# Kernel optimization log

Measured on AMD Instinct MI355X. Metric: run time of the kernel, lower is better.

The kernel has to match this reference:

```python
import jax, jax.numpy as jnp
import numpy as np

N = 50000      # nodes
E = 800000     # edges
G = 32         # graphs in batch
K = 16         # max current nodes per graph
F_IN = 128
HID = 64
HEADS = 4
NEG = -1e9
TEMPERATURE = 1.0


def setup_inputs() -> dict:
    key = jax.random.key(0)
    ks = jax.random.split(key, 16)
    inp = {
        "x": jax.random.normal(ks[0], (N, F_IN), dtype=jnp.float32),
        "edge_index": jax.random.randint(ks[1], (2, E), 0, N, dtype=jnp.int64) if jax.config.jax_enable_x64 else jax.random.randint(ks[1], (2, E), 0, N).astype(jnp.int32),
        "cur_nodes": jax.random.randint(ks[2], (G, K), 0, N).astype(jnp.int32),
        "cur_counts": jax.random.randint(ks[3], (G,), 0, K).astype(jnp.int32),
        "masks": jax.random.bernoulli(ks[4], 0.3, (G, N)),
        "W1": jax.random.normal(ks[5], (F_IN, HEADS * HID), dtype=jnp.float32) * 0.05,
        "att_src1": jax.random.normal(ks[6], (HEADS, HID), dtype=jnp.float32) * 0.05,
        "att_dst1": jax.random.normal(ks[7], (HEADS, HID), dtype=jnp.float32) * 0.05,
        "b1": jax.random.normal(ks[8], (HEADS * HID,), dtype=jnp.float32) * 0.05,
        "W2": jax.random.normal(ks[9], (HEADS * HID, HID), dtype=jnp.float32) * 0.05,
        "att_src2": jax.random.normal(ks[10], (1, HID), dtype=jnp.float32) * 0.05,
        "att_dst2": jax.random.normal(ks[11], (1, HID), dtype=jnp.float32) * 0.05,
        "b2": jax.random.normal(ks[12], (HID,), dtype=jnp.float32) * 0.05,
        "action_w": jax.random.normal(ks[13], (HID, 1), dtype=jnp.float32) * 0.01,
        "action_b": jnp.zeros((1,), dtype=jnp.float32),
        "stop_w": jax.random.normal(ks[14], (HID, 1), dtype=jnp.float32) * 0.01,
        "stop_b": jnp.zeros((1,), dtype=jnp.float32),
    }
    return inp


def gat_conv(x, src, dst, W, att_s, att_d, b, num_nodes):
    """PyG-style GATConv (add_self_loops already applied to src/dst)."""
    H, C = att_s.shape
    h = (x @ W).reshape(num_nodes, H, C)            # [N,H,C]
    a_s = jnp.sum(h * att_s[None], axis=-1)         # [N,H]
    a_d = jnp.sum(h * att_d[None], axis=-1)         # [N,H]
    e = jax.nn.leaky_relu(a_s[src] + a_d[dst], 0.2) # [E',H]
    m = jax.ops.segment_max(e, dst, num_segments=num_nodes)
    ex = jnp.exp(e - m[dst])
    denom = jax.ops.segment_sum(ex, dst, num_segments=num_nodes)
    coef = ex / denom[dst]                          # scatter-softmax over dst
    out = jax.ops.segment_sum(coef[:, :, None] * h[src], dst, num_segments=num_nodes)
    return out.reshape(num_nodes, H * C) + b


def reference(x, edge_index, cur_nodes, cur_counts, masks,
              W1, att_src1, att_dst1, b1, W2, att_src2, att_dst2, b2,
              action_w, action_b, stop_w, stop_b):
    num_nodes = x.shape[0]
    loops = jnp.arange(num_nodes, dtype=edge_index.dtype)
    src = jnp.concatenate([edge_index[0], loops])
    dst = jnp.concatenate([edge_index[1], loops])

    h = jax.nn.relu(gat_conv(x, src, dst, W1, att_src1, att_dst1, b1, num_nodes))
    h = gat_conv(h, src, dst, W2, att_src2, att_dst2, b2, num_nodes)  # [N,HID]

    node_scores = jnp.tanh(h @ action_w + action_b)[:, 0]             # [N]

    # per-graph masked gather-mean pooling over current nodes
    valid = (jnp.arange(K)[None, :] < cur_counts[:, None])            # [G,K]
    gathered = h[cur_nodes] * valid[:, :, None].astype(h.dtype)       # [G,K,HID]
    cnt = jnp.maximum(cur_counts, 1).astype(h.dtype)
    contexts = gathered.sum(axis=1) / cnt[:, None]                    # [G,HID]
    stop_scores = jnp.tanh(contexts @ stop_w + stop_b)                # [G,1]

    masked = jnp.where(masks, node_scores[None, :], NEG)              # [G,N]
    all_scores = jnp.concatenate([masked, stop_scores], axis=1) / TEMPERATURE
    probs = jax.nn.softmax(all_scores, axis=-1)                       # [G,N+1]

    stop = (cur_counts == 0)
    onehot = jnp.zeros((num_nodes + 1,), dtype=probs.dtype).at[num_nodes].set(1.0)
    return jnp.where(stop[:, None], onehot[None, :], probs)
```

## Files before the change

kernel.cpp:

```cpp
#include <hip/hip_runtime.h>
#include <hip/hip_runtime_api.h>

#define NNODES 50000
#define NEDGES 800000
#define GG 32
#define KCUR 16
#define FIN 128
#define HIDN 64
#define NHEADS 4
#define F1 256
#define NCHUNK 196
#define NBUCK 196
#define EPB 2048

typedef unsigned short u16;
typedef unsigned char u8;
typedef short bf8 __attribute__((ext_vector_type(8)));
typedef float f32x4 __attribute__((ext_vector_type(4)));
typedef float f32x2 __attribute__((ext_vector_type(2)));

__device__ __forceinline__ u16 f2bf(float f) {
    unsigned u = __float_as_uint(f);
    return (u16)((u + 0x7fffu + ((u >> 16) & 1u)) >> 16);
}
__device__ __forceinline__ float lrelu(float x) { return x > 0.f ? x : 0.2f * x; }
__device__ __forceinline__ unsigned pk4fp8(float a, float b, float c, float d) {
    unsigned u = __builtin_amdgcn_cvt_pk_fp8_f32(a, b, 0u, false);
    u = __builtin_amdgcn_cvt_pk_fp8_f32(c, d, u, true);
    return u;
}

__device__ __forceinline__ void fma16(uint4 hv, float ex, float* acc) {
    f32x2 c;
    c = __builtin_amdgcn_cvt_pk_f32_fp8(hv.x, false);
    acc[0]  = fmaf(ex, c.x, acc[0]);  acc[1]  = fmaf(ex, c.y, acc[1]);
    c = __builtin_amdgcn_cvt_pk_f32_fp8(hv.x, true);
    acc[2]  = fmaf(ex, c.x, acc[2]);  acc[3]  = fmaf(ex, c.y, acc[3]);
    c = __builtin_amdgcn_cvt_pk_f32_fp8(hv.y, false);
    acc[4]  = fmaf(ex, c.x, acc[4]);  acc[5]  = fmaf(ex, c.y, acc[5]);
    c = __builtin_amdgcn_cvt_pk_f32_fp8(hv.y, true);
    acc[6]  = fmaf(ex, c.x, acc[6]);  acc[7]  = fmaf(ex, c.y, acc[7]);
    c = __builtin_amdgcn_cvt_pk_f32_fp8(hv.z, false);
    acc[8]  = fmaf(ex, c.x, acc[8]);  acc[9]  = fmaf(ex, c.y, acc[9]);
    c = __builtin_amdgcn_cvt_pk_f32_fp8(hv.z, true);
    acc[10] = fmaf(ex, c.x, acc[10]); acc[11] = fmaf(ex, c.y, acc[11]);
    c = __builtin_amdgcn_cvt_pk_f32_fp8(hv.w, false);
    acc[12] = fmaf(ex, c.x, acc[12]); acc[13] = fmaf(ex, c.y, acc[13]);
    c = __builtin_amdgcn_cvt_pk_f32_fp8(hv.w, true);
    acc[14] = fmaf(ex, c.x, acc[14]); acc[15] = fmaf(ex, c.y, acc[15]);
}

__device__ __forceinline__ void fma8(uint2 hv, float ex, float* acc) {
    f32x2 c;
    c = __builtin_amdgcn_cvt_pk_f32_fp8(hv.x, false);
    acc[0] = fmaf(ex, c.x, acc[0]); acc[1] = fmaf(ex, c.y, acc[1]);
    c = __builtin_amdgcn_cvt_pk_f32_fp8(hv.x, true);
    acc[2] = fmaf(ex, c.x, acc[2]); acc[3] = fmaf(ex, c.y, acc[3]);
    c = __builtin_amdgcn_cvt_pk_f32_fp8(hv.y, false);
    acc[4] = fmaf(ex, c.x, acc[4]); acc[5] = fmaf(ex, c.y, acc[5]);
    c = __builtin_amdgcn_cvt_pk_f32_fp8(hv.y, true);
    acc[6] = fmaf(ex, c.x, acc[6]); acc[7] = fmaf(ex, c.y, acc[7]);
}

__global__ __launch_bounds__(256)
void pack_k(const float* __restrict__ W1, const float* __restrict__ W2,
            u16* __restrict__ W1p, u16* __restrict__ W2p)
{
    int idx = blockIdx.x * 256 + threadIdx.x;
    const float* src; u16* dst; int S, N, li;
    if (idx < 32768) { src = W1; dst = W1p; S = FIN / 32; N = F1; li = idx; }
    else if (idx < 49152) { src = W2; dst = W2p; S = F1 / 32; N = HIDN; li = idx - 32768; }
    else return;
    int j = li & 7, l = (li >> 3) & 63, rest = li >> 9;
    int s = rest % S, t = rest / S;
    int k = s * 32 + (l >> 4) * 8 + j;
    int n = t * 16 + (l & 15);
    dst[li] = f2bf(src[(size_t)k * N + n]);
}

__global__ __launch_bounds__(256)
void hist_k(const int* __restrict__ dst, int* __restrict__ deg)
{
    int e = blockIdx.x * 256 + threadIdx.x;
    if (e >= NEDGES) return;
    atomicAdd(&deg[dst[e]], 1);
}

__global__ __launch_bounds__(256)
void chunksum_k(const int* __restrict__ deg, int* __restrict__ csum)
{
    __shared__ int ws[4];
    int i = blockIdx.x * 256 + threadIdx.x;
    int v = (i < NNODES) ? deg[i] : 0;
#pragma unroll
    for (int o = 32; o; o >>= 1) v += __shfl_down(v, o);
    if ((threadIdx.x & 63) == 0) ws[threadIdx.x >> 6] = v;
    __syncthreads();
    if (threadIdx.x == 0) csum[blockIdx.x] = ws[0] + ws[1] + ws[2] + ws[3];
}

__global__ __launch_bounds__(256)
void expand_k(const int* __restrict__ deg, const int* __restrict__ csum,
              int* __restrict__ rowptr, int* __restrict__ bcur)
{
    __shared__ int ws[4], ws2[4];
    __shared__ int boff;
    int tid = threadIdx.x, lane = tid & 63, wid = tid >> 6;
    int v0 = (tid < blockIdx.x) ? csum[tid] : 0;
#pragma unroll
    for (int o = 32; o; o >>= 1) v0 += __shfl_down(v0, o);
    if (lane == 0) ws[wid] = v0;
    __syncthreads();
    if (tid == 0) boff = ws[0] + ws[1] + ws[2] + ws[3];
    __syncthreads();
    int i = blockIdx.x * 256 + tid;
    int v = (i < NNODES) ? deg[i] : 0;
    int x = v;
#pragma unroll
    for (int o = 1; o < 64; o <<= 1) {
        int y = __shfl_up(x, o);
        if (lane >= o) x += y;
    }
    if (lane == 63) ws2[wid] = x;
    __syncthreads();
    int off = boff;
    for (int w = 0; w < wid; w++) off += ws2[w];
    int excl = off + x - v;
    if (i < NNODES) {
        rowptr[i] = excl;
        if ((i & 255) == 0) bcur[i >> 8] = excl;
    }
    if (i == 0) rowptr[NNODES] = NEDGES;
}

__global__ __launch_bounds__(256)
void bin_k(const int* __restrict__ src, const int* __restrict__ dst,
           int* __restrict__ bcur, uint2* __restrict__ tmp)
{
    __shared__ int lcnt[NBUCK];
    __shared__ int lbase[NBUCK];
    int tid = threadIdx.x;
    int e0 = blockIdx.x * EPB;
    for (int i = tid; i < NBUCK; i += 256) lcnt[i] = 0;
    __syncthreads();
    int s_[8], d_[8], r_[8];
#pragma unroll
    for (int j = 0; j < 8; j++) {
        int e = e0 + j * 256 + tid;
        if (e < NEDGES) {
            s_[j] = src[e];
            d_[j] = dst[e];
            r_[j] = atomicAdd(&lcnt[d_[j] >> 8], 1);
        }
    }
    __syncthreads();
    for (int i = tid; i < NBUCK; i += 256)
        if (lcnt[i]) lbase[i] = atomicAdd(&bcur[i], lcnt[i]);
    __syncthreads();
#pragma unroll
    for (int j = 0; j < 8; j++) {
        int e = e0 + j * 256 + tid;
        if (e < NEDGES) {
            int b = d_[j] >> 8;
            tmp[lbase[b] + r_[j]] = make_uint2((unsigned)s_[j], (unsigned)d_[j]);
        }
    }
}

__global__ __launch_bounds__(1024)
void reorder_k(const int* __restrict__ rowptr, const uint2* __restrict__ tmp,
               int* __restrict__ csr)
{
    __shared__ int cur[256];
    int tid = threadIdx.x;
    int b = blockIdx.x;
    int n0 = b << 8;
    if (tid < 256) {
        int n = n0 + tid;
        cur[tid] = (n < NNODES) ? rowptr[n] : 0;
    }
    int base = rowptr[n0];
    int end = (b == NBUCK - 1) ? NEDGES : rowptr[n0 + 256];
    __syncthreads();
    for (int e = base + tid; e < end; e += 1024) {
        uint2 pr = tmp[e];
        int pos = atomicAdd(&cur[pr.y & 255], 1);
        csr[pos] = (int)pr.x;
    }
}

__global__ __launch_bounds__(256)
void gemm1_k(const float* __restrict__ X, const u16* __restrict__ Bp,
             const float* __restrict__ att_s, const float* __restrict__ att_d,
             u8* __restrict__ h1f8, float* __restrict__ as1, float* __restrict__ ad1)
{
    const int S = FIN / 32;
    int lane = threadIdx.x & 63, w = threadIdx.x >> 6;
    int m0 = blockIdx.x * 64;
    int row_in = lane & 15, kq = lane >> 4;
    f32x4 acc[4][4];
#pragma unroll
    for (int r = 0; r < 4; r++)
#pragma unroll
        for (int tt = 0; tt < 4; tt++) acc[r][tt] = (f32x4){0.f, 0.f, 0.f, 0.f};
    int R = (NNODES - m0) >> 4; if (R > 4) R = 4;

    for (int s = 0; s < S; s++) {
        bf8 bfrag[4];
#pragma unroll
        for (int tt = 0; tt < 4; tt++) {
            int t = w * 4 + tt;
            bfrag[tt] = *(const bf8*)(Bp + (((size_t)t * S + s) * 64 + lane) * 8);
        }
        int kb = s * 32 + kq * 8;
        bf8 af[4];
#pragma unroll
        for (int r = 0; r < 4; r++)
            if (r < R) {
                const float* xp = X + (size_t)(m0 + r * 16 + row_in) * FIN + kb;
                float4 x0 = *(const float4*)xp;
                float4 x1 = *(const float4*)(xp + 4);
                bf8 a;
                a[0] = (short)f2bf(x0.x); a[1] = (short)f2bf(x0.y);
                a[2] = (short)f2bf(x0.z); a[3] = (short)f2bf(x0.w);
                a[4] = (short)f2bf(x1.x); a[5] = (short)f2bf(x1.y);
                a[6] = (short)f2bf(x1.z); a[7] = (short)f2bf(x1.w);
                af[r] = a;
            }
#pragma unroll
        for (int r = 0; r < 4; r++)
            if (r < R)
#pragma unroll
                for (int tt = 0; tt < 4; tt++)
                    acc[r][tt] = __builtin_amdgcn_mfma_f32_16x16x32_bf16(bfrag[tt], af[r], acc[r][tt], 0, 0, 0);
    }
    float attS[16], attD[16];
#pragma unroll
    for (int tt = 0; tt < 4; tt++)
#pragma unroll
        for (int v = 0; v < 4; v++) {
            attS[tt * 4 + v] = att_s[w * 64 + tt * 16 + kq * 4 + v];
            attD[tt * 4 + v] = att_d[w * 64 + tt * 16 + kq * 4 + v];
        }
#pragma unroll
    for (int r = 0; r < 4; r++) {
        if (r >= R) break;
        int node = m0 + r * 16 + row_in;
        float pa = 0.f, pd = 0.f;
#pragma unroll
        for (int tt = 0; tt < 4; tt++) {
            unsigned u = pk4fp8(acc[r][tt][0], acc[r][tt][1], acc[r][tt][2], acc[r][tt][3]);
            *(unsigned*)(h1f8 + (size_t)node * F1 + (w * 4 + tt) * 16 + kq * 4) = u;
#pragma unroll
            for (int v = 0; v < 4; v++) {
                pa = fmaf(acc[r][tt][v], attS[tt * 4 + v], pa);
                pd = fmaf(acc[r][tt][v], attD[tt * 4 + v], pd);
            }
        }
        pa += __shfl_xor(pa, 16); pa += __shfl_xor(pa, 32);
        pd += __shfl_xor(pd, 16); pd += __shfl_xor(pd, 32);
        if (kq == 0) { as1[node * 4 + w] = pa; ad1[node * 4 + w] = pd; }
    }
}

__global__ __launch_bounds__(256)
void gagg1_gemm2(const int* __restrict__ rowptr, const int* __restrict__ csr,
                 const float* __restrict__ as1, const float* __restrict__ ad1,
                 const u8* __restrict__ h1f8, const float* __restrict__ b1,
                 const u16* __restrict__ W2p,
                 const float* __restrict__ att_s, const float* __restrict__ att_d,
                 u8* __restrict__ h2f8, float* __restrict__ as2, float* __restrict__ ad2)
{
    __shared__ unsigned rows[16 * 128];
    __shared__ float asl[4][16], adl[4][16];
    int tid = threadIdx.x;
    int wid = tid >> 6, lane = tid & 63;
    int q = lane >> 4, li = lane & 15;
    int dl = wid * 4 + q;
    int d0 = blockIdx.x * 16;
    int d = d0 + dl;
    int beg = rowptr[d];
    int tot = rowptr[d + 1] - beg + 1;
    int h = li >> 2;
    int c0 = li << 4;
    const int* rowm = csr + beg - 1;
    float adh = ad1[d * 4 + h];
    float den = 0.f;
    float acc[16];
#pragma unroll
    for (int j = 0; j < 16; j++) acc[j] = 0.f;

    int s0 = d;
    int s1 = (1 < tot) ? rowm[1] : d;
    int s2 = (2 < tot) ? rowm[2] : d;
    int s3 = (3 < tot) ? rowm[3] : d;
    int p = 0;
    while (p < tot) {
        float av0 = as1[((unsigned)s0 << 2) + h];
        float av1 = as1[((unsigned)s1 << 2) + h];
        float av2 = as1[((unsigned)s2 << 2) + h];
        float av3 = as1[((unsigned)s3 << 2) + h];
        uint4 h0 = *(const uint4*)(h1f8 + ((unsigned)s0 << 8) + c0);
        uint4 h1 = *(const uint4*)(h1f8 + ((unsigned)s1 << 8) + c0);
        uint4 h2 = *(const uint4*)(h1f8 + ((unsigned)s2 << 8) + c0);
        uint4 h3 = *(const uint4*)(h1f8 + ((unsigned)s3 << 8) + c0);
        int np = p + 4;
        int n0 = (np     < tot) ? rowm[np]     : d;
        int n1 = (np + 1 < tot) ? rowm[np + 1] : d;
        int n2 = (np + 2 < tot) ? rowm[np + 2] : d;
        int n3 = (np + 3 < tot) ? rowm[np + 3] : d;
        float e0 = __expf(lrelu(av0 + adh));
        float e1 = (p + 1 < tot) ? __expf(lrelu(av1 + adh)) : 0.f;
        float e2 = (p + 2 < tot) ? __expf(lrelu(av2 + adh)) : 0.f;
        float e3 = (p + 3 < tot) ? __expf(lrelu(av3 + adh)) : 0.f;
        den += e0 + e1 + e2 + e3;
        fma16(h0, e0, acc);
        fma16(h1, e1, acc);
        fma16(h2, e2, acc);
        fma16(h3, e3, acc);
        s0 = n0; s1 = n1; s2 = n2; s3 = n3;
        p = np;
    }

    {
        float rden = 1.f / den;
        float4 b0 = *(const float4*)(b1 + c0);
        float4 b4 = *(const float4*)(b1 + c0 + 4);
        float4 b8 = *(const float4*)(b1 + c0 + 8);
        float4 bc = *(const float4*)(b1 + c0 + 12);
        float bb[16] = {b0.x, b0.y, b0.z, b0.w, b4.x, b4.y, b4.z, b4.w,
                        b8.x, b8.y, b8.z, b8.w, bc.x, bc.y, bc.z, bc.w};
        unsigned r[8];
#pragma unroll
        for (int jj = 0; jj < 8; jj++) {
            float lo = fmaxf(fmaf(acc[2 * jj],     rden, bb[2 * jj]),     0.f);
            float hi = fmaxf(fmaf(acc[2 * jj + 1], rden, bb[2 * jj + 1]), 0.f);
            asm("v_cvt_pk_bf16_f32 %0, %1, %2" : "=v"(r[jj]) : "v"(lo), "v"(hi));
        }
        unsigned* rb = rows + dl * 128;
        int g0 = (2 * li) ^ (dl & 7);
        int g1 = (2 * li + 1) ^ (dl & 7);
        *(uint4*)(rb + g0 * 4) = make_uint4(r[0], r[1], r[2], r[3]);
        *(uint4*)(rb + g1 * 4) = make_uint4(r[4], r[5], r[6], r[7]);
    }
    __syncthreads();

    int row_in = li, kq = q;
    f32x4 acc2 = (f32x4){0.f, 0.f, 0.f, 0.f};
#pragma unroll
    for (int s = 0; s < 8; s++) {
        bf8 bfrag = *(const bf8*)(W2p + (((size_t)wid * 8 + s) * 64 + lane) * 8);
        int g = (4 * s + kq) ^ (row_in & 7);
        bf8 af = *(const bf8*)(rows + row_in * 128 + g * 4);
        acc2 = __builtin_amdgcn_mfma_f32_16x16x32_bf16(bfrag, af, acc2, 0, 0, 0);
    }
    int node = d0 + row_in;
    unsigned u = pk4fp8(acc2[0], acc2[1], acc2[2], acc2[3]);
    *(unsigned*)(h2f8 + (size_t)node * HIDN + wid * 16 + kq * 4) = u;
    float pa = 0.f, pd = 0.f;
#pragma unroll
    for (int v = 0; v < 4; v++) {
        pa = fmaf(acc2[v], att_s[wid * 16 + kq * 4 + v], pa);
        pd = fmaf(acc2[v], att_d[wid * 16 + kq * 4 + v], pd);
    }
    pa += __shfl_xor(pa, 16); pa += __shfl_xor(pa, 32);
    pd += __shfl_xor(pd, 16); pd += __shfl_xor(pd, 32);
    if (kq == 0) { asl[wid][row_in] = pa; adl[wid][row_in] = pd; }
    __syncthreads();
    if (tid < 16) {
        as2[d0 + tid] = asl[0][tid] + asl[1][tid] + asl[2][tid] + asl[3][tid];
        ad2[d0 + tid] = adl[0][tid] + adl[1][tid] + adl[2][tid] + adl[3][tid];
    }
}

__global__ __launch_bounds__(256)
void gagg2(const int* __restrict__ rowptr, const int* __restrict__ csr,
           const float* __restrict__ as2, const float* __restrict__ ad2,
           const u8* __restrict__ h2f8, const float* __restrict__ b2,
           const float* __restrict__ aw, const float* __restrict__ ab,
           float* __restrict__ outp, float* __restrict__ scores)
{
    int wid = threadIdx.x >> 6, lane = threadIdx.x & 63;
    int d = blockIdx.x * 4 + wid;
    if (d >= NNODES) return;
    int beg = rowptr[d];
    int tot = rowptr[d + 1] - beg + 1;
    int g8 = lane >> 3;
    int li = lane & 7;
    int c0 = li << 3;
    const int* rowm = csr + beg - 1;
    float adh = ad2[d];
    float den = 0.f;
    float acc[8];
#pragma unroll
    for (int j = 0; j < 8; j++) acc[j] = 0.f;

    int p = g8;
    while (p + 8 < tot) {
        int sa = (p == 0) ? d : rowm[p];
        int sb = rowm[p + 8];
        float ava = as2[sa], avb = as2[sb];
        uint2 ha = *(const uint2*)(h2f8 + ((unsigned)sa << 6) + c0);
        uint2 hb = *(const uint2*)(h2f8 + ((unsigned)sb << 6) + c0);
        float exa = __expf(lrelu(ava + adh));
        den += exa;
        fma8(ha, exa, acc);
        float exb = __expf(lrelu(avb + adh));
        den += exb;
        fma8(hb, exb, acc);
        p += 16;
    }
    if (p < tot) {
        int s = (p == 0) ? d : rowm[p];
        float av = as2[s];
        uint2 hv = *(const uint2*)(h2f8 + ((unsigned)s << 6) + c0);
        float ex = __expf(lrelu(av + adh));
        den += ex;
        fma8(hv, ex, acc);
    }

    den += __shfl_xor(den, 8); den += __shfl_xor(den, 16); den += __shfl_xor(den, 32);
#pragma unroll
    for (int j = 0; j < 8; j++) {
        acc[j] += __shfl_xor(acc[j], 8);
        acc[j] += __shfl_xor(acc[j], 16);
        acc[j] += __shfl_xor(acc[j], 32);
    }

    float rden = 1.f / den;
    float4 blo = *(const float4*)(b2 + c0);
    float4 bhi = *(const float4*)(b2 + c0 + 4);
    float o0 = fmaf(acc[0], rden, blo.x);
    float o1 = fmaf(acc[1], rden, blo.y);
    float o2 = fmaf(acc[2], rden, blo.z);
    float o3 = fmaf(acc[3], rden, blo.w);
    float o4 = fmaf(acc[4], rden, bhi.x);
    float o5 = fmaf(acc[5], rden, bhi.y);
    float o6 = fmaf(acc[6], rden, bhi.z);
    float o7 = fmaf(acc[7], rden, bhi.w);
    if (lane < 8) {
        *(float4*)(outp + (size_t)d * HIDN + c0) = make_float4(o0, o1, o2, o3);
        *(float4*)(outp + (size_t)d * HIDN + c0 + 4) = make_float4(o4, o5, o6, o7);
    }
    float4 alo = *(const float4*)(aw + c0);
    float4 ahi = *(const float4*)(aw + c0 + 4);
    float p_ = o0 * alo.x + o1 * alo.y + o2 * alo.z + o3 * alo.w
             + o4 * ahi.x + o5 * ahi.y + o6 * ahi.z + o7 * ahi.w;
    p_ += __shfl_xor(p_, 1); p_ += __shfl_xor(p_, 2); p_ += __shfl_xor(p_, 4);
    if (lane == 0) scores[d] = tanhf(p_ + ab[0]);
}

__global__ __launch_bounds__(256)
void partials_k(const float* __restrict__ scores, const int* __restrict__ masks,
                float* __restrict__ pmax, float* __restrict__ psum)
{
    __shared__ float lm[4], ls[4];
    int g = blockIdx.y;
    float m = -3.0e38f, s = 0.f;
    for (int n = blockIdx.x * 256 + threadIdx.x; n < NNODES; n += gridDim.x * 256) {
        if (masks[(size_t)g * NNODES + n]) {
            float v = scores[n];
            if (v > m) { s = s * __expf(m - v) + 1.f; m = v; }
            else s += __expf(v - m);
        }
    }
#pragma unroll
    for (int o = 1; o < 64; o <<= 1) {
        float om = __shfl_xor(m, o), os = __shfl_xor(s, o);
        float M = fmaxf(m, om);
        s = s * __expf(m - M) + os * __expf(om - M);
        m = M;
    }
    if ((threadIdx.x & 63) == 0) { lm[threadIdx.x >> 6] = m; ls[threadIdx.x >> 6] = s; }
    __syncthreads();
    if (threadIdx.x == 0) {
        float M = m, S = s;
        for (int w_ = 1; w_ < 4; w_++) {
            float M2 = fmaxf(M, lm[w_]);
            S = S * __expf(M - M2) + ls[w_] * __expf(lm[w_] - M2);
            M = M2;
        }
        pmax[g * 64 + blockIdx.x] = M;
        psum[g * 64 + blockIdx.x] = S;
    }
}

__global__ __launch_bounds__(64)
void combine_k(const float* __restrict__ hf, const int* __restrict__ cur_nodes,
               const int* __restrict__ cur_counts, const float* __restrict__ sw,
               const float* __restrict__ sb,
               const float* __restrict__ pmax, const float* __restrict__ psum,
               float* __restrict__ gmax, float* __restrict__ gsum,
               float* __restrict__ stops)
{
    int g = blockIdx.x, tid = threadIdx.x;
    int cnt = cur_counts[g];
    float s = 0.f;
    for (int k = 0; k < KCUR; k++)
        if (k < cnt) s += hf[(size_t)cur_nodes[g * KCUR + k] * HIDN + tid];
    float ctx = s / (float)(cnt > 1 ? cnt : 1);
    float p = ctx * sw[tid];
#pragma unroll
    for (int o = 1; o < 64; o <<= 1) p += __shfl_xor(p, o);
    float stop = tanhf(p + sb[0]);

    float m = pmax[g * 64 + tid], sm = psum[g * 64 + tid];
#pragma unroll
    for (int o = 1; o < 64; o <<= 1) {
        float om = __shfl_xor(m, o), os = __shfl_xor(sm, o);
        float M = fmaxf(m, om);
        sm = sm * __expf(m - M) + os * __expf(om - M);
        m = M;
    }
    if (tid == 0) {
        float M2 = fmaxf(m, stop);
        float S2 = sm * __expf(m - M2) + __expf(stop - M2);
        gmax[g] = M2; gsum[g] = S2; stops[g] = stop;
    }
}

__global__ __launch_bounds__(256)
void write_k(const float* __restrict__ scores, const int* __restrict__ masks,
             const float* __restrict__ gmax, const float* __restrict__ gsum,
             const float* __restrict__ stops, const int* __restrict__ cur_counts,
             float* __restrict__ out)
{
    int g = blockIdx.y;
    int j = blockIdx.x * 256 + threadIdx.x;
    if (j > NNODES) return;
    float v;
    if (cur_counts[g] == 0) {
        v = (j == NNODES) ? 1.f : 0.f;
    } else {
        float m = gmax[g];
        float Z = gsum[g];
        if (j == NNODES) v = __expf(stops[g] - m) / Z;
        else v = masks[(size_t)g * NNODES + j] ? __expf(scores[j] - m) / Z : 0.f;
    }
    out[(size_t)g * (NNODES + 1) + j] = v;
}

extern "C" void kernel_launch(void* const* d_in, const int* in_sizes, int n_in,
                              void* d_out, int out_size, void* d_ws, size_t ws_size,
                              hipStream_t stream) {
    const float* x        = (const float*)d_in[0];
    const int* ei         = (const int*)d_in[1];
    const int* cur_nodes  = (const int*)d_in[2];
    const int* cur_counts = (const int*)d_in[3];
    const int* masks      = (const int*)d_in[4];
    const float* W1       = (const float*)d_in[5];
    const float* att_s1   = (const float*)d_in[6];
    const float* att_d1   = (const float*)d_in[7];
    const float* b1       = (const float*)d_in[8];
    const float* W2       = (const float*)d_in[9];
    const float* att_s2   = (const float*)d_in[10];
    const float* att_d2   = (const float*)d_in[11];
    const float* b2       = (const float*)d_in[12];
    const float* action_w = (const float*)d_in[13];
    const float* action_b = (const float*)d_in[14];
    const float* stop_w   = (const float*)d_in[15];
    const float* stop_b   = (const float*)d_in[16];
    float* out = (float*)d_out;

    const int* srcp = ei;
    const int* dstp = ei + NEDGES;

    int* deg = (int*)d_ws;
    char* zend = (char*)(deg + NNODES);
    size_t zbytes = zend - (char*)d_ws;
    int* csum   = (int*)zend;
    int* rowptr = csum + 256;
    int* bcur   = rowptr + NNODES + 4;
    int* csr    = bcur + 256;
    u16* W1p    = (u16*)(csr + NEDGES);
    u16* W2p    = W1p + 32768;
    u8*  h1f8   = (u8*)(W2p + 16384);
    u8*  h2f8   = h1f8 + (size_t)NNODES * F1;
    float* as1  = (float*)(h2f8 + (size_t)NNODES * HIDN);
    float* ad1  = as1 + (size_t)NNODES * 4;
    float* as2  = ad1 + (size_t)NNODES * 4;
    float* ad2  = as2 + NNODES;
    float* hf   = ad2 + NNODES;
    float* scores = hf + (size_t)NNODES * HIDN;
    float* stops  = scores + NNODES;
    float* pmax = stops + GG;
    float* psum = pmax + GG * 64;
    float* gmax = psum + GG * 64;
    float* gsum = gmax + GG;
    size_t total = (char*)(gsum + GG) - (char*)d_ws;
    if (total > ws_size) return;

    uint2* tmp = (uint2*)hf;

    auto cdiv = [](long long a, long long b) { return (int)((a + b - 1) / b); };

    (void)hipMemsetAsync(deg, 0, zbytes, stream);

    hist_k<<<cdiv(NEDGES, 256), 256, 0, stream>>>(dstp, deg);
    chunksum_k<<<NCHUNK, 256, 0, stream>>>(deg, csum);
    expand_k<<<NCHUNK, 256, 0, stream>>>(deg, csum, rowptr, bcur);
    bin_k<<<cdiv(NEDGES, EPB), 256, 0, stream>>>(srcp, dstp, bcur, tmp);
    reorder_k<<<NBUCK, 1024, 0, stream>>>(rowptr, tmp, csr);

    pack_k<<<192, 256, 0, stream>>>(W1, W2, W1p, W2p);

    gemm1_k<<<cdiv(NNODES, 64), 256, 0, stream>>>(x, W1p, att_s1, att_d1, h1f8, as1, ad1);

    gagg1_gemm2<<<NNODES / 16, 256, 0, stream>>>(rowptr, csr, as1, ad1, h1f8, b1,
                                                 W2p, att_s2, att_d2, h2f8, as2, ad2);

    gagg2<<<cdiv(NNODES, 4), 256, 0, stream>>>(rowptr, csr, as2, ad2, h2f8, b2,
                                               action_w, action_b, hf, scores);

    partials_k<<<dim3(64, GG), 256, 0, stream>>>(scores, masks, pmax, psum);
    combine_k<<<GG, 64, 0, stream>>>(hf, cur_nodes, cur_counts, stop_w, stop_b,
                                     pmax, psum, gmax, gsum, stops);
    write_k<<<dim3(cdiv(NNODES + 1, 256), GG), 256, 0, stream>>>(scores, masks, gmax, gsum,
                                                                 stops, cur_counts, out);
}
```

Measured before the change: 282.4 us.

## Drop degree-histogram CSR prepass and max-free softmax with atomic sums

Replaces the hist/chunksum/expand prepass with fixed-capacity per-bucket binning, where reorder_k computes bucket offsets and per-node row pointers itself. The memset is folded into the weight-pack kernel, so three kernels and a memset are gone. The softmax drops the running max because scores are tanh-bounded, and accumulates per-graph sums with atomics instead of max/sum partials. This risks silent edge loss if a bucket exceeds BCAP (6000 slots against about 4096 expected edges per bucket), and adds float atomics that make the sums order-dependent.

```diff
diff --git a/kernel.cpp b/kernel.cpp
--- a/kernel.cpp
+++ b/kernel.cpp
@@ -9,8 +9,8 @@
 #define HIDN 64
 #define NHEADS 4
 #define F1 256
-#define NCHUNK 196
 #define NBUCK 196
+#define BCAP 6000
 #define EPB 2048
 
 typedef unsigned short u16;
@@ -63,10 +63,16 @@
 }
 
 __global__ __launch_bounds__(256)
-void pack_k(const float* __restrict__ W1, const float* __restrict__ W2,
-            u16* __restrict__ W1p, u16* __restrict__ W2p)
-{
-    int idx = blockIdx.x * 256 + threadIdx.x;
+void init_k(const float* __restrict__ W1, const float* __restrict__ W2,
+            u16* __restrict__ W1p, u16* __restrict__ W2p,
+            int* __restrict__ bctr, float* __restrict__ gsum)
+{
+    int tid = threadIdx.x;
+    if (blockIdx.x == 0) {
+        bctr[tid] = 0;
+        if (tid < GG) gsum[tid] = 0.f;
+    }
+    int idx = blockIdx.x * 256 + tid;
     const float* src; u16* dst; int S, N, li;
     if (idx < 32768) { src = W1; dst = W1p; S = FIN / 32; N = F1; li = idx; }
     else if (idx < 49152) { src = W2; dst = W2p; S = F1 / 32; N = HIDN; li = idx - 32768; }
@@ -79,63 +85,8 @@
 }
 
 __global__ __launch_bounds__(256)
-void hist_k(const int* __restrict__ dst, int* __restrict__ deg)
-{
-    int e = blockIdx.x * 256 + threadIdx.x;
-    if (e >= NEDGES) return;
-    atomicAdd(&deg[dst[e]], 1);
-}
-
-__global__ __launch_bounds__(256)
-void chunksum_k(const int* __restrict__ deg, int* __restrict__ csum)
-{
-    __shared__ int ws[4];
-    int i = blockIdx.x * 256 + threadIdx.x;
-    int v = (i < NNODES) ? deg[i] : 0;
-#pragma unroll
-    for (int o = 32; o; o >>= 1) v += __shfl_down(v, o);
-    if ((threadIdx.x & 63) == 0) ws[threadIdx.x >> 6] = v;
-    __syncthreads();
-    if (threadIdx.x == 0) csum[blockIdx.x] = ws[0] + ws[1] + ws[2] + ws[3];
-}
-
-__global__ __launch_bounds__(256)
-void expand_k(const int* __restrict__ deg, const int* __restrict__ csum,
-              int* __restrict__ rowptr, int* __restrict__ bcur)
-{
-    __shared__ int ws[4], ws2[4];
-    __shared__ int boff;
-    int tid = threadIdx.x, lane = tid & 63, wid = tid >> 6;
-    int v0 = (tid < blockIdx.x) ? csum[tid] : 0;
-#pragma unroll
-    for (int o = 32; o; o >>= 1) v0 += __shfl_down(v0, o);
-    if (lane == 0) ws[wid] = v0;
-    __syncthreads();
-    if (tid == 0) boff = ws[0] + ws[1] + ws[2] + ws[3];
-    __syncthreads();
-    int i = blockIdx.x * 256 + tid;
-    int v = (i < NNODES) ? deg[i] : 0;
-    int x = v;
-#pragma unroll
-    for (int o = 1; o < 64; o <<= 1) {
-        int y = __shfl_up(x, o);
-        if (lane >= o) x += y;
-    }
-    if (lane == 63) ws2[wid] = x;
-    __syncthreads();
-    int off = boff;
-    for (int w = 0; w < wid; w++) off += ws2[w];
-    int excl = off + x - v;
-    if (i < NNODES) {
-        rowptr[i] = excl;
-        if ((i & 255) == 0) bcur[i >> 8] = excl;
-    }
-    if (i == 0) rowptr[NNODES] = NEDGES;
-}
-
-__global__ __launch_bounds__(256)
 void bin_k(const int* __restrict__ src, const int* __restrict__ dst,
-           int* __restrict__ bcur, uint2* __restrict__ tmp)
+           int* __restrict__ bctr, uint2* __restrict__ tmp)
 {
     __shared__ int lcnt[NBUCK];
     __shared__ int lbase[NBUCK];
@@ -155,36 +106,75 @@
     }
     __syncthreads();
     for (int i = tid; i < NBUCK; i += 256)
-        if (lcnt[i]) lbase[i] = atomicAdd(&bcur[i], lcnt[i]);
+        if (lcnt[i]) lbase[i] = atomicAdd(&bctr[i], lcnt[i]);
     __syncthreads();
 #pragma unroll
     for (int j = 0; j < 8; j++) {
         int e = e0 + j * 256 + tid;
         if (e < NEDGES) {
             int b = d_[j] >> 8;
-            tmp[lbase[b] + r_[j]] = make_uint2((unsigned)s_[j], (unsigned)d_[j]);
+            int pos = lbase[b] + r_[j];
+            if (pos < BCAP)
+                tmp[(size_t)b * BCAP + pos] = make_uint2((unsigned)s_[j], (unsigned)d_[j]);
         }
     }
 }
 
 __global__ __launch_bounds__(1024)
-void reorder_k(const int* __restrict__ rowptr, const uint2* __restrict__ tmp,
-               int* __restrict__ csr)
-{
-    __shared__ int cur[256];
-    int tid = threadIdx.x;
-    int b = blockIdx.x;
-    int n0 = b << 8;
+void reorder_k(const int* __restrict__ bctr, const uint2* __restrict__ tmp,
+               int* __restrict__ rowptr, int* __restrict__ csr)
+{
+    __shared__ int hist[256];
+    __shared__ int excl[256];
+    __shared__ int ws[16];
+    __shared__ int ws2[4];
+    __shared__ int sbase;
+    int tid = threadIdx.x, b = blockIdx.x;
+    int lane = tid & 63, wid = tid >> 6;
+
+    int v0 = (tid < b) ? bctr[tid] : 0;
+#pragma unroll
+    for (int o = 32; o; o >>= 1) v0 += __shfl_down(v0, o);
+    if (lane == 0) ws[wid] = v0;
+    if (tid < 256) hist[tid] = 0;
+    __syncthreads();
+    if (tid == 0) {
+        int s = 0;
+        for (int w = 0; w < 16; w++) s += ws[w];
+        sbase = s;
+    }
+    int cnt = bctr[b];
+    const uint2* pairs = tmp + (size_t)b * BCAP;
+    for (int i = tid; i < cnt; i += 1024)
+        atomicAdd(&hist[pairs[i].y & 255], 1);
+    __syncthreads();
+
     if (tid < 256) {
-        int n = n0 + tid;
-        cur[tid] = (n < NNODES) ? rowptr[n] : 0;
-    }
-    int base = rowptr[n0];
-    int end = (b == NBUCK - 1) ? NEDGES : rowptr[n0 + 256];
-    __syncthreads();
-    for (int e = base + tid; e < end; e += 1024) {
-        uint2 pr = tmp[e];
-        int pos = atomicAdd(&cur[pr.y & 255], 1);
+        int v = hist[tid];
+        int x = v;
+#pragma unroll
+        for (int o = 1; o < 64; o <<= 1) {
+            int y = __shfl_up(x, o);
+            if (lane >= o) x += y;
+        }
+        excl[tid] = x - v;
+        if (lane == 63) ws2[wid] = x;
+    }
+    __syncthreads();
+    if (tid < 256) {
+        int off = sbase;
+        for (int w = 0; w < wid; w++) off += ws2[w];
+        int e = off + excl[tid];
+        int n = (b << 8) + tid;
+        if (n < NNODES) rowptr[n] = e;
+        hist[tid] = e;
+    }
+    if (b == NBUCK - 1 && tid == 0) rowptr[NNODES] = NEDGES;
+    __syncthreads();
+
+    for (int i = tid; i < cnt; i += 1024) {
+        uint2 pr = pairs[i];
+        int pos = atomicAdd(&hist[pr.y & 255], 1);
         csr[pos] = (int)pr.x;
     }
 }
@@ -452,46 +442,25 @@
 
 __global__ __launch_bounds__(256)
 void partials_k(const float* __restrict__ scores, const int* __restrict__ masks,
-                float* __restrict__ pmax, float* __restrict__ psum)
-{
-    __shared__ float lm[4], ls[4];
+                float* __restrict__ gsum)
+{
+    __shared__ float ls[4];
     int g = blockIdx.y;
-    float m = -3.0e38f, s = 0.f;
-    for (int n = blockIdx.x * 256 + threadIdx.x; n < NNODES; n += gridDim.x * 256) {
-        if (masks[(size_t)g * NNODES + n]) {
-            float v = scores[n];
-            if (v > m) { s = s * __expf(m - v) + 1.f; m = v; }
-            else s += __expf(v - m);
-        }
-    }
-#pragma unroll
-    for (int o = 1; o < 64; o <<= 1) {
-        float om = __shfl_xor(m, o), os = __shfl_xor(s, o);
-        float M = fmaxf(m, om);
-        s = s * __expf(m - M) + os * __expf(om - M);
-        m = M;
-    }
-    if ((threadIdx.x & 63) == 0) { lm[threadIdx.x >> 6] = m; ls[threadIdx.x >> 6] = s; }
-    __syncthreads();
-    if (threadIdx.x == 0) {
-        float M = m, S = s;
-        for (int w_ = 1; w_ < 4; w_++) {
-            float M2 = fmaxf(M, lm[w_]);
-            S = S * __expf(M - M2) + ls[w_] * __expf(lm[w_] - M2);
-            M = M2;
-        }
-        pmax[g * 64 + blockIdx.x] = M;
-        psum[g * 64 + blockIdx.x] = S;
-    }
+    float s = 0.f;
+    for (int n = blockIdx.x * 256 + threadIdx.x; n < NNODES; n += gridDim.x * 256)
+        if (masks[(size_t)g * NNODES + n]) s += __expf(scores[n]);
+#pragma unroll
+    for (int o = 32; o; o >>= 1) s += __shfl_down(s, o);
+    if ((threadIdx.x & 63) == 0) ls[threadIdx.x >> 6] = s;
+    __syncthreads();
+    if (threadIdx.x == 0) atomicAdd(&gsum[g], ls[0] + ls[1] + ls[2] + ls[3]);
 }
 
 __global__ __launch_bounds__(64)
 void combine_k(const float* __restrict__ hf, const int* __restrict__ cur_nodes,
                const int* __restrict__ cur_counts, const float* __restrict__ sw,
                const float* __restrict__ sb,
-               const float* __restrict__ pmax, const float* __restrict__ psum,
-               float* __restrict__ gmax, float* __restrict__ gsum,
-               float* __restrict__ stops)
+               float* __restrict__ gsum, float* __restrict__ stops)
 {
     int g = blockIdx.x, tid = threadIdx.x;
     int cnt = cur_counts[g];
@@ -502,28 +471,17 @@
     float p = ctx * sw[tid];
 #pragma unroll
     for (int o = 1; o < 64; o <<= 1) p += __shfl_xor(p, o);
-    float stop = tanhf(p + sb[0]);
-
-    float m = pmax[g * 64 + tid], sm = psum[g * 64 + tid];
-#pragma unroll
-    for (int o = 1; o < 64; o <<= 1) {
-        float om = __shfl_xor(m, o), os = __shfl_xor(sm, o);
-        float M = fmaxf(m, om);
-        sm = sm * __expf(m - M) + os * __expf(om - M);
-        m = M;
-    }
     if (tid == 0) {
-        float M2 = fmaxf(m, stop);
-        float S2 = sm * __expf(m - M2) + __expf(stop - M2);
-        gmax[g] = M2; gsum[g] = S2; stops[g] = stop;
+        float stop = tanhf(p + sb[0]);
+        stops[g] = stop;
+        atomicAdd(&gsum[g], __expf(stop));
     }
 }
 
 __global__ __launch_bounds__(256)
 void write_k(const float* __restrict__ scores, const int* __restrict__ masks,
-             const float* __restrict__ gmax, const float* __restrict__ gsum,
-             const float* __restrict__ stops, const int* __restrict__ cur_counts,
-             float* __restrict__ out)
+             const float* __restrict__ gsum, const float* __restrict__ stops,
+             const int* __restrict__ cur_counts, float* __restrict__ out)
 {
     int g = blockIdx.y;
     int j = blockIdx.x * 256 + threadIdx.x;
@@ -532,10 +490,9 @@
     if (cur_counts[g] == 0) {
         v = (j == NNODES) ? 1.f : 0.f;
     } else {
-        float m = gmax[g];
-        float Z = gsum[g];
-        if (j == NNODES) v = __expf(stops[g] - m) / Z;
-        else v = masks[(size_t)g * NNODES + j] ? __expf(scores[j] - m) / Z : 0.f;
+        float rz = 1.f / gsum[g];
+        if (j == NNODES) v = __expf(stops[g]) * rz;
+        else v = masks[(size_t)g * NNODES + j] ? __expf(scores[j]) * rz : 0.f;
     }
     out[(size_t)g * (NNODES + 1) + j] = v;
 }
@@ -565,13 +522,9 @@
     const int* srcp = ei;
     const int* dstp = ei + NEDGES;
 
-    int* deg = (int*)d_ws;
-    char* zend = (char*)(deg + NNODES);
-    size_t zbytes = zend - (char*)d_ws;
-    int* csum   = (int*)zend;
-    int* rowptr = csum + 256;
-    int* bcur   = rowptr + NNODES + 4;
-    int* csr    = bcur + 256;
+    int* rowptr = (int*)d_ws;
+    int* bctr   = rowptr + NNODES + 4;
+    int* csr    = bctr + 256;
     u16* W1p    = (u16*)(csr + NEDGES);
     u16* W2p    = W1p + 32768;
     u8*  h1f8   = (u8*)(W2p + 16384);
@@ -583,10 +536,7 @@
     float* hf   = ad2 + NNODES;
     float* scores = hf + (size_t)NNODES * HIDN;
     float* stops  = scores + NNODES;
-    float* pmax = stops + GG;
-    float* psum = pmax + GG * 64;
-    float* gmax = psum + GG * 64;
-    float* gsum = gmax + GG;
+    float* gsum = stops + GG;
     size_t total = (char*)(gsum + GG) - (char*)d_ws;
     if (total > ws_size) return;
 
@@ -594,15 +544,11 @@
 
     auto cdiv = [](long long a, long long b) { return (int)((a + b - 1) / b); };
 
-    (void)hipMemsetAsync(deg, 0, zbytes, stream);
-
-    hist_k<<<cdiv(NEDGES, 256), 256, 0, stream>>>(dstp, deg);
-    chunksum_k<<<NCHUNK, 256, 0, stream>>>(deg, csum);
-    expand_k<<<NCHUNK, 256, 0, stream>>>(deg, csum, rowptr, bcur);
-    bin_k<<<cdiv(NEDGES, EPB), 256, 0, stream>>>(srcp, dstp, bcur, tmp);
-    reorder_k<<<NBUCK, 1024, 0, stream>>>(rowptr, tmp, csr);
-
-    pack_k<<<192, 256, 0, stream>>>(W1, W2, W1p, W2p);
+    init_k<<<192, 256, 0, stream>>>(W1, W2, W1p, W2p, bctr, gsum);
+
+    bin_k<<<cdiv(NEDGES, EPB), 256, 0, stream>>>(srcp, dstp, bctr, tmp);
+
+    reorder_k<<<NBUCK, 1024, 0, stream>>>(bctr, tmp, rowptr, csr);
 
     gemm1_k<<<cdiv(NNODES, 64), 256, 0, stream>>>(x, W1p, att_s1, att_d1, h1f8, as1, ad1);
 
@@ -612,9 +558,11 @@
     gagg2<<<cdiv(NNODES, 4), 256, 0, stream>>>(rowptr, csr, as2, ad2, h2f8, b2,
                                                action_w, action_b, hf, scores);
 
-    partials_k<<<dim3(64, GG), 256, 0, stream>>>(scores, masks, pmax, psum);
+    partials_k<<<dim3(64, GG), 256, 0, stream>>>(scores, masks, gsum);
+
     combine_k<<<GG, 64, 0, stream>>>(hf, cur_nodes, cur_counts, stop_w, stop_b,
-                                     pmax, psum, gmax, gsum, stops);
-    write_k<<<dim3(cdiv(NNODES + 1, 256), GG), 256, 0, stream>>>(scores, masks, gmax, gsum,
+                                     gsum, stops);
+
+    write_k<<<dim3(cdiv(NNODES + 1, 256), GG), 256, 0, stream>>>(scores, masks, gsum,
                                                                  stops, cur_counts, out);
 }
```

After: 251.4 us. 11.0% less time.
